# Kernel optimization log

Hardware: AMD Instinct MI355X
Metric: run time of the kernel (lower is better)

The kernel has to match this reference:

```python
import jax, jax.numpy as jnp
import numpy as np

TAU = 2.0
EPS = 1e-5
SG_ALPHA = 4.0  # spikingjelly default Sigmoid surrogate alpha


@jax.custom_vjp
def heaviside(x):
    return (x >= 0.0).astype(x.dtype)

def _heaviside_fwd(x):
    return heaviside(x), x

def _heaviside_bwd(x, g):
    s = jax.nn.sigmoid(SG_ALPHA * x)
    return (g * SG_ALPHA * s * (1.0 - s),)

heaviside.defvjp(_heaviside_fwd, _heaviside_bwd)


def lif(x_seq, v_th):
    """Multi-step LIF, hard reset to 0, detach_reset=True. x_seq: (T, ...)."""
    def step(v, x_t):
        v = v + (x_t - v) / TAU
        s = heaviside(v - v_th)
        v = v * (1.0 - jax.lax.stop_gradient(s))  # detached hard reset
        return v, s
    _, spikes = jax.lax.scan(step, jnp.zeros_like(x_seq[0]), x_seq)
    return spikes


def bn(y, gamma, beta, mean, var):
    # y: (T, B, C, N); inference-mode BatchNorm1d over channel dim
    inv = gamma / jnp.sqrt(var + EPS)
    return y * inv[None, None, :, None] + (beta - mean * inv)[None, None, :, None]


def setup_inputs() -> dict:
    key = jax.random.key(0)
    ks = jax.random.split(key, 8)
    T, B, C, H, W = 4, 32, 256, 32, 32
    d = {
        "x": jax.random.normal(ks[0], (T, B, C, H, W), jnp.float32),
        "q_w": jax.random.normal(ks[1], (C, C), jnp.float32) * (1.0 / np.sqrt(C)),
        "q_gamma": jnp.ones((C,), jnp.float32),
        "q_beta": jnp.zeros((C,), jnp.float32),
        "q_mean": jnp.zeros((C,), jnp.float32),
        "q_var": jnp.ones((C,), jnp.float32),
        "k_w": jax.random.normal(ks[2], (C, C), jnp.float32) * (1.0 / np.sqrt(C)),
        "k_gamma": jnp.ones((C,), jnp.float32),
        "k_beta": jnp.zeros((C,), jnp.float32),
        "k_mean": jnp.zeros((C,), jnp.float32),
        "k_var": jnp.ones((C,), jnp.float32),
        "p_w": jax.random.normal(ks[3], (C, C), jnp.float32) * (1.0 / np.sqrt(C)),
        "p_b": jnp.zeros((C,), jnp.float32),
        "p_gamma": jnp.ones((C,), jnp.float32),
        "p_beta": jnp.zeros((C,), jnp.float32),
        "p_mean": jnp.zeros((C,), jnp.float32),
        "p_var": jnp.ones((C,), jnp.float32),
    }
    return d


def reference(x, q_w, q_gamma, q_beta, q_mean, q_var,
              k_w, k_gamma, k_beta, k_mean, k_var,
              p_w, p_b, p_gamma, p_beta, p_mean, p_var):
    T, B, C, H, W = x.shape
    num_heads = 8
    dh = C // num_heads
    N = H * W
    xs = x.reshape(T, B, C, N)

    # Q branch: 1x1 conv (C x C matmul) -> BN -> LIF
    q = bn(jnp.einsum('oc,tbcn->tbon', q_w, xs), q_gamma, q_beta, q_mean, q_var)
    q_spikes = lif(q, 1.0)                                # (T,B,C,N)
    q_h = q_spikes.reshape(T, B, num_heads, dh, N)

    # K branch
    k = bn(jnp.einsum('oc,tbcn->tbon', k_w, xs), k_gamma, k_beta, k_mean, k_var)
    k_spikes = lif(k, 1.0)
    k_h = k_spikes.reshape(T, B, num_heads, dh, N)

    # channel-sum pooled Q per head -> attn LIF (v_th=0.5) -> elementwise mult with K
    q_sum = jnp.sum(q_h, axis=3, keepdims=True)           # (T,B,h,1,N)
    attn = lif(q_sum, 0.5)
    x_one = attn * k_h                                    # (T,B,h,dh,N)

    # projection: 1x1 conv with bias -> BN -> LIF
    xo = x_one.reshape(T, B, C, N)
    xo = jnp.einsum('oc,tbcn->tbon', p_w, xo) + p_b[None, None, :, None]
    xo = bn(xo, p_gamma, p_beta, p_mean, p_var).reshape(T, B, C, H, W)
    x_final = lif(xo, 1.0)
    return x_final
```

## Files before the change

kernel.cpp:

```cpp
#include <hip/hip_runtime.h>
#include <cstdint>
#include <cstddef>

#define T_DIM 4
#define B_DIM 32
#define C_DIM 256
#define N_DIM 1024
#define NHEAD 8
#define DHEAD 32
#define NWRD 32

__device__ __forceinline__ float lif_step(float& v, float x, float vth) {
    v = __fadd_rn(v, __fmul_rn(__fsub_rn(x, v), 0.5f));
    const float s = (v >= vth) ? 1.0f : 0.0f;
    if (s != 0.0f) v = 0.0f;
    return s;
}

__device__ __forceinline__ void async_copy16(const float* g, float* l) {
    __builtin_amdgcn_global_load_lds(
        (const __attribute__((address_space(1))) unsigned int*)g,
        (__attribute__((address_space(3))) unsigned int*)l, 16, 0, 0);
}

#define FMA_ROW(r, av)                                \
    acc[(r)*8+0] = fmaf(av, b0.x, acc[(r)*8+0]);      \
    acc[(r)*8+1] = fmaf(av, b0.y, acc[(r)*8+1]);      \
    acc[(r)*8+2] = fmaf(av, b0.z, acc[(r)*8+2]);      \
    acc[(r)*8+3] = fmaf(av, b0.w, acc[(r)*8+3]);      \
    acc[(r)*8+4] = fmaf(av, b1.x, acc[(r)*8+4]);      \
    acc[(r)*8+5] = fmaf(av, b1.y, acc[(r)*8+5]);      \
    acc[(r)*8+6] = fmaf(av, b1.z, acc[(r)*8+6]);      \
    acc[(r)*8+7] = fmaf(av, b1.w, acc[(r)*8+7]);

__global__ __launch_bounds__(256) void k_transpose(
    const float* __restrict__ qw, const float* __restrict__ kw,
    const float* __restrict__ pw, float* __restrict__ wqk_t,
    float* __restrict__ p_t)
{
    const int i = blockIdx.x * 256 + threadIdx.x;
    if (i < C_DIM * 512) {
        const int k = i >> 9, col = i & 511;
        const int h = col >> 6, j = col & 63;
        wqk_t[i] = (j < 32) ? qw[(size_t)(h * 32 + j) * C_DIM + k]
                            : kw[(size_t)(h * 32 + j - 32) * C_DIM + k];
    } else {
        const int i2 = i - C_DIM * 512;
        const int k = i2 >> 8, c = i2 & 255;
        p_t[i2] = pw[(size_t)c * C_DIM + k];
    }
}

__global__ __launch_bounds__(256, 4) void k_qk(
    const float* __restrict__ x, const float* __restrict__ wqk,
    const float* __restrict__ qg, const float* __restrict__ qbeta,
    const float* __restrict__ qmean, const float* __restrict__ qvar,
    const float* __restrict__ kg, const float* __restrict__ kbeta,
    const float* __restrict__ kmean, const float* __restrict__ kvar,
    uint32_t* __restrict__ xbits)
{
    __shared__ float w_lds[32 * 64];
    __shared__ float x_lds[32 * 128];
    float*    qsum_lds = x_lds;
    float*    attn_lds = x_lds + 128;
    uint32_t* pack_lds = (uint32_t*)(x_lds + 256);

    const int tid = threadIdx.x;
    const int h = blockIdx.x, nt = blockIdx.y, b = blockIdx.z;
    const int n0g = nt * 128;

    const int  mg = tid >> 4;
    const int  m0 = mg << 2;
    const int  ng = tid & 15;
    const int  n0 = ng << 2;
    const bool is_q = (mg < 8);

    float inv4[4], bias4[4];
    {
        const float* g  = is_q ? qg    : kg;
        const float* be = is_q ? qbeta : kbeta;
        const float* me = is_q ? qmean : kmean;
        const float* va = is_q ? qvar  : kvar;
        const int cb = h * DHEAD + (is_q ? m0 : (m0 - 32));
        #pragma unroll
        for (int i = 0; i < 4; i++) {
            const float iv = __fdiv_rn(g[cb + i], __fsqrt_rn(__fadd_rn(va[cb + i], 1e-5f)));
            inv4[i]  = iv;
            bias4[i] = __fsub_rn(be[cb + i], __fmul_rn(me[cb + i], iv));
        }
    }

    const int wk = tid >> 4;
    const int wm = (tid & 15) << 2;
    const int xk = tid >> 5;
    const int xc = (tid & 31) << 2;
    const float* wgp = wqk + h * 64 + wm;

    float vstate[32];
    #pragma unroll
    for (int i = 0; i < 32; i++) vstate[i] = 0.0f;
    float v_attn = 0.0f;

    for (int t = 0; t < T_DIM; ++t) {
        float acc[32];
        #pragma unroll
        for (int i = 0; i < 32; i++) acc[i] = 0.0f;

        const float* xgp = x + (size_t)(t * B_DIM + b) * C_DIM * N_DIM + n0g + xc;

        for (int c = 0; c < 8; ++c) {
            const int kk = c * 32;
            __syncthreads();
            async_copy16(wgp + (size_t)(kk      + wk) * 512, w_lds + tid * 4);
            async_copy16(wgp + (size_t)(kk + 16 + wk) * 512, w_lds + 1024 + tid * 4);
            #pragma unroll
            for (int r = 0; r < 4; r++)
                async_copy16(xgp + (size_t)(kk + r * 8 + xk) * N_DIM,
                             x_lds + r * 1024 + tid * 4);
            __syncthreads();
            #pragma unroll 4
            for (int k = 0; k < 32; k++) {
                const float4 a  = *(const float4*)(w_lds + k * 64 + m0);
                const float4 b0 = *(const float4*)(x_lds + k * 128 + n0);
                const float4 b1 = *(const float4*)(x_lds + k * 128 + 64 + n0);
                FMA_ROW(0, a.x)
                FMA_ROW(1, a.y)
                FMA_ROW(2, a.z)
                FMA_ROW(3, a.w)
            }
        }

        #pragma unroll
        for (int r = 0; r < 4; r++) {
            #pragma unroll
            for (int j = 0; j < 8; j++) {
                const float y = __fadd_rn(__fmul_rn(acc[r * 8 + j], inv4[r]), bias4[r]);
                acc[r * 8 + j] = lif_step(vstate[r * 8 + j], y, 1.0f);
            }
        }

        __syncthreads();
        if (tid < 128) qsum_lds[tid] = 0.0f; else pack_lds[tid - 128] = 0u;
        __syncthreads();

        if (is_q) {
            #pragma unroll
            for (int j = 0; j < 8; j++) {
                const int col = (j < 4) ? (n0 + j) : (64 + n0 + (j - 4));
                const float cs = acc[j] + acc[8 + j] + acc[16 + j] + acc[24 + j];
                atomicAdd(&qsum_lds[col], cs);
            }
        }
        __syncthreads();
        if (tid < 128) attn_lds[tid] = lif_step(v_attn, qsum_lds[tid], 0.5f);
        __syncthreads();

        if (!is_q) {
            #pragma unroll
            for (int r = 0; r < 4; r++) {
                const int krow = (mg - 8) * 4 + r;
                #pragma unroll
                for (int ci = 0; ci < 2; ci++) {
                    uint32_t nib = 0;
                    #pragma unroll
                    for (int jj = 0; jj < 4; jj++) {
                        const int col = ci * 64 + n0 + jj;
                        if (acc[r * 8 + ci * 4 + jj] != 0.0f && attn_lds[col] != 0.0f)
                            nib |= (1u << jj);
                    }
                    if (nib) {
                        const int word = ci * 2 + (ng >> 3);
                        const int shf  = (ng & 7) * 4;
                        atomicOr(&pack_lds[krow * 4 + word], nib << shf);
                    }
                }
            }
        }
        __syncthreads();
        if (tid < 128) {
            const int krow = tid >> 2, word = tid & 3;
            const int ch = h * DHEAD + krow;
            xbits[((size_t)(t * B_DIM + b) * C_DIM + ch) * NWRD + nt * 4 + word]
                = pack_lds[tid];
        }
    }
}

__global__ __launch_bounds__(256, 4) void k_proj(
    const uint32_t* __restrict__ xbits, const float* __restrict__ pt,
    const float* __restrict__ pbias, const float* __restrict__ pg,
    const float* __restrict__ pbeta, const float* __restrict__ pmean,
    const float* __restrict__ pvar, float* __restrict__ out)
{
    __shared__ float w_lds[32 * 64];
    __shared__ float x_lds[32 * 128];

    const int tid = threadIdx.x;
    const int mt = blockIdx.x, nt = blockIdx.y, b = blockIdx.z;
    const int n0g = nt * 128;
    const int c0  = mt * 64;

    const int mg = tid >> 4, m0 = mg << 2;
    const int ng = tid & 15, n0 = ng << 2;

    float inv4[4], bias4[4], pb4[4];
    #pragma unroll
    for (int i = 0; i < 4; i++) {
        const int ch = c0 + m0 + i;
        const float iv = __fdiv_rn(pg[ch], __fsqrt_rn(__fadd_rn(pvar[ch], 1e-5f)));
        inv4[i]  = iv;
        bias4[i] = __fsub_rn(pbeta[ch], __fmul_rn(pmean[ch], iv));
        pb4[i]   = pbias[ch];
    }

    const int wk = tid >> 4;
    const int wm = (tid & 15) << 2;
    const float* wgp = pt + c0 + wm;

    const int usel = nt * 4 + ((tid & 31) >> 3);
    const int shf  = (tid & 7) * 4;
    const int urow = tid >> 5;

    float vstate[32];
    #pragma unroll
    for (int i = 0; i < 32; i++) vstate[i] = 0.0f;

    for (int t = 0; t < T_DIM; ++t) {
        float acc[32];
        #pragma unroll
        for (int i = 0; i < 32; i++) acc[i] = 0.0f;

        const uint32_t* xg = xbits + (size_t)(t * B_DIM + b) * C_DIM * NWRD;

        uint32_t u[4];
        #pragma unroll
        for (int r = 0; r < 4; r++)
            u[r] = xg[(size_t)(r * 8 + urow) * NWRD + usel];

        for (int c = 0; c < 8; ++c) {
            __syncthreads();
            #pragma unroll
            for (int r = 0; r < 4; r++) {
                const uint32_t bits = (u[r] >> shf) & 0xFu;
                float4 f;
                f.x = (bits & 1u)        ? 1.0f : 0.0f;
                f.y = ((bits >> 1) & 1u) ? 1.0f : 0.0f;
                f.z = ((bits >> 2) & 1u) ? 1.0f : 0.0f;
                f.w = ((bits >> 3) & 1u) ? 1.0f : 0.0f;
                *(float4*)(x_lds + r * 1024 + tid * 4) = f;
            }
            async_copy16(wgp + (size_t)(c * 32      + wk) * 256, w_lds + tid * 4);
            async_copy16(wgp + (size_t)(c * 32 + 16 + wk) * 256, w_lds + 1024 + tid * 4);
            __syncthreads();
            if (c + 1 < 8) {
                #pragma unroll
                for (int r = 0; r < 4; r++)
                    u[r] = xg[(size_t)((c + 1) * 32 + r * 8 + urow) * NWRD + usel];
            }
            #pragma unroll 4
            for (int k = 0; k < 32; k++) {
                const float4 a  = *(const float4*)(w_lds + k * 64 + m0);
                const float4 b0 = *(const float4*)(x_lds + k * 128 + n0);
                const float4 b1 = *(const float4*)(x_lds + k * 128 + 64 + n0);
                FMA_ROW(0, a.x)
                FMA_ROW(1, a.y)
                FMA_ROW(2, a.z)
                FMA_ROW(3, a.w)
            }
        }

        #pragma unroll
        for (int r = 0; r < 4; r++) {
            const int ch = c0 + m0 + r;
            float* ob = out + ((size_t)(t * B_DIM + b) * C_DIM + ch) * N_DIM + n0g;
            float4 oA, oB;
            float oAv[4], oBv[4];
            #pragma unroll
            for (int j = 0; j < 8; j++) {
                float y = __fadd_rn(acc[r * 8 + j], pb4[r]);
                y = __fadd_rn(__fmul_rn(y, inv4[r]), bias4[r]);
                const float s = lif_step(vstate[r * 8 + j], y, 1.0f);
                if (j < 4) oAv[j] = s; else oBv[j - 4] = s;
            }
            oA.x = oAv[0]; oA.y = oAv[1]; oA.z = oAv[2]; oA.w = oAv[3];
            oB.x = oBv[0]; oB.y = oBv[1]; oB.z = oBv[2]; oB.w = oBv[3];
            *(float4*)(ob + n0)      = oA;
            *(float4*)(ob + 64 + n0) = oB;
        }
    }
}

extern "C" void kernel_launch(void* const* d_in, const int* in_sizes, int n_in,
                              void* d_out, int out_size, void* d_ws, size_t ws_size,
                              hipStream_t stream) {
    const float* x    = (const float*)d_in[0];
    const float* q_w  = (const float*)d_in[1];
    const float* q_g  = (const float*)d_in[2];
    const float* q_b  = (const float*)d_in[3];
    const float* q_m  = (const float*)d_in[4];
    const float* q_v  = (const float*)d_in[5];
    const float* k_w  = (const float*)d_in[6];
    const float* k_g  = (const float*)d_in[7];
    const float* k_b  = (const float*)d_in[8];
    const float* k_m  = (const float*)d_in[9];
    const float* k_v  = (const float*)d_in[10];
    const float* p_w  = (const float*)d_in[11];
    const float* p_b  = (const float*)d_in[12];
    const float* p_g  = (const float*)d_in[13];
    const float* p_be = (const float*)d_in[14];
    const float* p_m  = (const float*)d_in[15];
    const float* p_v  = (const float*)d_in[16];

    float*    wqk_t = (float*)d_ws;
    float*    p_t   = (float*)((char*)d_ws + 524288);
    uint32_t* xbits = (uint32_t*)((char*)d_ws + 786432);
    float*    out   = (float*)d_out;

    k_transpose<<<768, 256, 0, stream>>>(q_w, k_w, p_w, wqk_t, p_t);

    dim3 g1(NHEAD, N_DIM / 128, B_DIM);
    k_qk<<<g1, 256, 0, stream>>>(x, wqk_t, q_g, q_b, q_m, q_v,
                                 k_g, k_b, k_m, k_v, xbits);

    dim3 g2(C_DIM / 64, N_DIM / 128, B_DIM);
    k_proj<<<g2, 256, 0, stream>>>(xbits, p_t, p_b, p_g, p_be, p_m, p_v, out);
}
```

Measured before the change: 877.6 us.

## Enlarge register tiles to 8x8 per thread, processing two heads per block

Each thread's micro-tile grows from 4x8 to 8x8 outputs in both the QK and projection GEMM kernels, so each block covers 128 output channels (two heads in k_qk) and the grid is halved. The goal is better arithmetic intensity per LDS load and fewer redundant reloads of x tiles across head blocks. BN constants move to shared memory, and the bit-unpack loader in k_proj is reorganised around the new tile. The cost is much higher register pressure (64 accumulators plus 64 LIF states), occupancy lowered to 3 blocks per SM, and fewer blocks in the grid.

Measured after the change: 829.0 us. 1.06x faster.

```diff
diff --git a/kernel.cpp b/kernel.cpp
--- a/kernel.cpp
+++ b/kernel.cpp
@@ -32,6 +32,16 @@
     acc[(r)*8+5] = fmaf(av, b1.y, acc[(r)*8+5]);      \
     acc[(r)*8+6] = fmaf(av, b1.z, acc[(r)*8+6]);      \
     acc[(r)*8+7] = fmaf(av, b1.w, acc[(r)*8+7]);
+
+#define FMA_8x8()        \
+    FMA_ROW(0, a0.x)     \
+    FMA_ROW(1, a0.y)     \
+    FMA_ROW(2, a0.z)     \
+    FMA_ROW(3, a0.w)     \
+    FMA_ROW(4, a1.x)     \
+    FMA_ROW(5, a1.y)     \
+    FMA_ROW(6, a1.z)     \
+    FMA_ROW(7, a1.w)
 
 __global__ __launch_bounds__(256) void k_transpose(
     const float* __restrict__ qw, const float* __restrict__ kw,
@@ -51,7 +61,7 @@
     }
 }
 
-__global__ __launch_bounds__(256, 4) void k_qk(
+__global__ __launch_bounds__(256, 3) void k_qk(
     const float* __restrict__ x, const float* __restrict__ wqk,
     const float* __restrict__ qg, const float* __restrict__ qbeta,
     const float* __restrict__ qmean, const float* __restrict__ qvar,
@@ -59,229 +69,237 @@
     const float* __restrict__ kmean, const float* __restrict__ kvar,
     uint32_t* __restrict__ xbits)
 {
-    __shared__ float w_lds[32 * 64];
+    __shared__ float w_lds[32 * 128];
     __shared__ float x_lds[32 * 128];
+    __shared__ float inv_lds[128];
+    __shared__ float bias_lds[128];
     float*    qsum_lds = x_lds;
-    float*    attn_lds = x_lds + 128;
-    uint32_t* pack_lds = (uint32_t*)(x_lds + 256);
+    float*    attn_lds = x_lds + 256;
+    uint32_t* pack_lds = (uint32_t*)(x_lds + 512);
 
     const int tid = threadIdx.x;
-    const int h = blockIdx.x, nt = blockIdx.y, b = blockIdx.z;
+    const int hp = blockIdx.x, nt = blockIdx.y, b = blockIdx.z;
     const int n0g = nt * 128;
 
-    const int  mg = tid >> 4;
-    const int  m0 = mg << 2;
-    const int  ng = tid & 15;
-    const int  n0 = ng << 2;
-    const bool is_q = (mg < 8);
-
-    float inv4[4], bias4[4];
-    {
-        const float* g  = is_q ? qg    : kg;
-        const float* be = is_q ? qbeta : kbeta;
-        const float* me = is_q ? qmean : kmean;
-        const float* va = is_q ? qvar  : kvar;
-        const int cb = h * DHEAD + (is_q ? m0 : (m0 - 32));
+    const int  mg   = tid >> 4;
+    const int  m0   = mg << 3;
+    const int  ng   = tid & 15;
+    const int  n0   = ng << 2;
+    const int  hsel = mg >> 3;
+    const bool is_q = ((mg & 7) < 4);
+
+    if (tid < 128) {
+        const int m = tid;
+        const int hs = m >> 6, j = m & 63;
+        const int h = hp * 2 + hs;
+        const bool q = (j < 32);
+        const float* g  = q ? qg    : kg;
+        const float* be = q ? qbeta : kbeta;
+        const float* me = q ? qmean : kmean;
+        const float* va = q ? qvar  : kvar;
+        const int ch = h * DHEAD + (q ? j : j - 32);
+        const float iv = __fdiv_rn(g[ch], __fsqrt_rn(__fadd_rn(va[ch], 1e-5f)));
+        inv_lds[m]  = iv;
+        bias_lds[m] = __fsub_rn(be[ch], __fmul_rn(me[ch], iv));
+    }
+
+    const int skl  = tid >> 5;
+    const int scol = (tid & 31) << 2;
+    const float* wgp = wqk + (size_t)skl * 512 + hp * 128 + scol;
+
+    float vstate[64];
+    #pragma unroll
+    for (int i = 0; i < 64; i++) vstate[i] = 0.0f;
+    float v_attn = 0.0f;
+
+    for (int t = 0; t < T_DIM; ++t) {
+        float acc[64];
         #pragma unroll
-        for (int i = 0; i < 4; i++) {
-            const float iv = __fdiv_rn(g[cb + i], __fsqrt_rn(__fadd_rn(va[cb + i], 1e-5f)));
-            inv4[i]  = iv;
-            bias4[i] = __fsub_rn(be[cb + i], __fmul_rn(me[cb + i], iv));
-        }
-    }
-
-    const int wk = tid >> 4;
-    const int wm = (tid & 15) << 2;
-    const int xk = tid >> 5;
-    const int xc = (tid & 31) << 2;
-    const float* wgp = wqk + h * 64 + wm;
-
-    float vstate[32];
-    #pragma unroll
-    for (int i = 0; i < 32; i++) vstate[i] = 0.0f;
-    float v_attn = 0.0f;
-
-    for (int t = 0; t < T_DIM; ++t) {
-        float acc[32];
-        #pragma unroll
-        for (int i = 0; i < 32; i++) acc[i] = 0.0f;
-
-        const float* xgp = x + (size_t)(t * B_DIM + b) * C_DIM * N_DIM + n0g + xc;
+        for (int i = 0; i < 64; i++) acc[i] = 0.0f;
+
+        const float* xgp = x + ((size_t)(t * B_DIM + b) * C_DIM + skl) * N_DIM
+                           + n0g + scol;
 
         for (int c = 0; c < 8; ++c) {
             const int kk = c * 32;
             __syncthreads();
-            async_copy16(wgp + (size_t)(kk      + wk) * 512, w_lds + tid * 4);
-            async_copy16(wgp + (size_t)(kk + 16 + wk) * 512, w_lds + 1024 + tid * 4);
-            #pragma unroll
-            for (int r = 0; r < 4; r++)
-                async_copy16(xgp + (size_t)(kk + r * 8 + xk) * N_DIM,
-                             x_lds + r * 1024 + tid * 4);
+            #pragma unroll
+            for (int r = 0; r < 4; r++) {
+                async_copy16(wgp + (size_t)(kk + r * 8) * 512, w_lds + r * 1024 + tid * 4);
+                async_copy16(xgp + (size_t)(kk + r * 8) * N_DIM, x_lds + r * 1024 + tid * 4);
+            }
             __syncthreads();
-            #pragma unroll 4
+            #pragma unroll 2
             for (int k = 0; k < 32; k++) {
-                const float4 a  = *(const float4*)(w_lds + k * 64 + m0);
+                const float4 a0 = *(const float4*)(w_lds + k * 128 + m0);
+                const float4 a1 = *(const float4*)(w_lds + k * 128 + m0 + 4);
                 const float4 b0 = *(const float4*)(x_lds + k * 128 + n0);
                 const float4 b1 = *(const float4*)(x_lds + k * 128 + 64 + n0);
-                FMA_ROW(0, a.x)
-                FMA_ROW(1, a.y)
-                FMA_ROW(2, a.z)
-                FMA_ROW(3, a.w)
+                FMA_8x8()
             }
         }
 
         #pragma unroll
-        for (int r = 0; r < 4; r++) {
+        for (int r = 0; r < 8; r++) {
+            const float iv = inv_lds[m0 + r];
+            const float bs = bias_lds[m0 + r];
             #pragma unroll
             for (int j = 0; j < 8; j++) {
-                const float y = __fadd_rn(__fmul_rn(acc[r * 8 + j], inv4[r]), bias4[r]);
+                const float y = __fadd_rn(__fmul_rn(acc[r * 8 + j], iv), bs);
                 acc[r * 8 + j] = lif_step(vstate[r * 8 + j], y, 1.0f);
             }
         }
 
         __syncthreads();
-        if (tid < 128) qsum_lds[tid] = 0.0f; else pack_lds[tid - 128] = 0u;
+        qsum_lds[tid] = 0.0f;
+        pack_lds[tid] = 0u;
         __syncthreads();
 
         if (is_q) {
             #pragma unroll
             for (int j = 0; j < 8; j++) {
                 const int col = (j < 4) ? (n0 + j) : (64 + n0 + (j - 4));
-                const float cs = acc[j] + acc[8 + j] + acc[16 + j] + acc[24 + j];
-                atomicAdd(&qsum_lds[col], cs);
-            }
-        }
-        __syncthreads();
-        if (tid < 128) attn_lds[tid] = lif_step(v_attn, qsum_lds[tid], 0.5f);
+                float cs = acc[j];
+                #pragma unroll
+                for (int r = 1; r < 8; r++) cs += acc[r * 8 + j];
+                atomicAdd(&qsum_lds[hsel * 128 + col], cs);
+            }
+        }
+        __syncthreads();
+        attn_lds[tid] = lif_step(v_attn, qsum_lds[tid], 0.5f);
         __syncthreads();
 
         if (!is_q) {
             #pragma unroll
-            for (int r = 0; r < 4; r++) {
-                const int krow = (mg - 8) * 4 + r;
+            for (int r = 0; r < 8; r++) {
+                const int krow = ((mg & 7) - 4) * 8 + r;
                 #pragma unroll
                 for (int ci = 0; ci < 2; ci++) {
                     uint32_t nib = 0;
                     #pragma unroll
                     for (int jj = 0; jj < 4; jj++) {
                         const int col = ci * 64 + n0 + jj;
-                        if (acc[r * 8 + ci * 4 + jj] != 0.0f && attn_lds[col] != 0.0f)
+                        if (acc[r * 8 + ci * 4 + jj] != 0.0f &&
+                            attn_lds[hsel * 128 + col] != 0.0f)
                             nib |= (1u << jj);
                     }
                     if (nib) {
                         const int word = ci * 2 + (ng >> 3);
                         const int shf  = (ng & 7) * 4;
-                        atomicOr(&pack_lds[krow * 4 + word], nib << shf);
+                        atomicOr(&pack_lds[hsel * 128 + krow * 4 + word], nib << shf);
                     }
                 }
             }
         }
         __syncthreads();
-        if (tid < 128) {
-            const int krow = tid >> 2, word = tid & 3;
-            const int ch = h * DHEAD + krow;
+        {
+            const int hs2  = tid >> 7;
+            const int rem  = tid & 127;
+            const int krow = rem >> 2, word = rem & 3;
+            const int ch = (hp * 2 + hs2) * DHEAD + krow;
             xbits[((size_t)(t * B_DIM + b) * C_DIM + ch) * NWRD + nt * 4 + word]
                 = pack_lds[tid];
         }
     }
 }
 
-__global__ __launch_bounds__(256, 4) void k_proj(
+__global__ __launch_bounds__(256, 3) void k_proj(
     const uint32_t* __restrict__ xbits, const float* __restrict__ pt,
     const float* __restrict__ pbias, const float* __restrict__ pg,
     const float* __restrict__ pbeta, const float* __restrict__ pmean,
     const float* __restrict__ pvar, float* __restrict__ out)
 {
-    __shared__ float w_lds[32 * 64];
+    __shared__ float w_lds[32 * 128];
     __shared__ float x_lds[32 * 128];
+    __shared__ float inv_lds[128];
+    __shared__ float bias_lds[128];
+    __shared__ float pb_lds[128];
 
     const int tid = threadIdx.x;
     const int mt = blockIdx.x, nt = blockIdx.y, b = blockIdx.z;
     const int n0g = nt * 128;
-    const int c0  = mt * 64;
-
-    const int mg = tid >> 4, m0 = mg << 2;
+    const int c0  = mt * 128;
+
+    const int mg = tid >> 4, m0 = mg << 3;
     const int ng = tid & 15, n0 = ng << 2;
 
-    float inv4[4], bias4[4], pb4[4];
+    if (tid < 128) {
+        const int ch = c0 + tid;
+        const float iv = __fdiv_rn(pg[ch], __fsqrt_rn(__fadd_rn(pvar[ch], 1e-5f)));
+        inv_lds[tid]  = iv;
+        bias_lds[tid] = __fsub_rn(pbeta[ch], __fmul_rn(pmean[ch], iv));
+        pb_lds[tid]   = pbias[ch];
+    }
+
+    const int skl  = tid >> 5;
+    const int scol = (tid & 31) << 2;
+    const float* wgp = pt + (size_t)skl * 256 + c0 + scol;
+
+    const int urow = tid >> 3, cg = tid & 7;
+    const int wsel = nt * 4 + (cg >> 1);
+    const int ushf = (cg & 1) * 16;
+    float* xw = x_lds + tid * 16;
+
+    float vstate[64];
     #pragma unroll
-    for (int i = 0; i < 4; i++) {
-        const int ch = c0 + m0 + i;
-        const float iv = __fdiv_rn(pg[ch], __fsqrt_rn(__fadd_rn(pvar[ch], 1e-5f)));
-        inv4[i]  = iv;
-        bias4[i] = __fsub_rn(pbeta[ch], __fmul_rn(pmean[ch], iv));
-        pb4[i]   = pbias[ch];
-    }
-
-    const int wk = tid >> 4;
-    const int wm = (tid & 15) << 2;
-    const float* wgp = pt + c0 + wm;
-
-    const int usel = nt * 4 + ((tid & 31) >> 3);
-    const int shf  = (tid & 7) * 4;
-    const int urow = tid >> 5;
-
-    float vstate[32];
-    #pragma unroll
-    for (int i = 0; i < 32; i++) vstate[i] = 0.0f;
+    for (int i = 0; i < 64; i++) vstate[i] = 0.0f;
 
     for (int t = 0; t < T_DIM; ++t) {
-        float acc[32];
+        float acc[64];
         #pragma unroll
-        for (int i = 0; i < 32; i++) acc[i] = 0.0f;
+        for (int i = 0; i < 64; i++) acc[i] = 0.0f;
 
         const uint32_t* xg = xbits + (size_t)(t * B_DIM + b) * C_DIM * NWRD;
 
-        uint32_t u[4];
-        #pragma unroll
-        for (int r = 0; r < 4; r++)
-            u[r] = xg[(size_t)(r * 8 + urow) * NWRD + usel];
+        uint32_t u = xg[(size_t)urow * NWRD + wsel];
 
         for (int c = 0; c < 8; ++c) {
             __syncthreads();
-            #pragma unroll
-            for (int r = 0; r < 4; r++) {
-                const uint32_t bits = (u[r] >> shf) & 0xFu;
-                float4 f;
-                f.x = (bits & 1u)        ? 1.0f : 0.0f;
-                f.y = ((bits >> 1) & 1u) ? 1.0f : 0.0f;
-                f.z = ((bits >> 2) & 1u) ? 1.0f : 0.0f;
-                f.w = ((bits >> 3) & 1u) ? 1.0f : 0.0f;
-                *(float4*)(x_lds + r * 1024 + tid * 4) = f;
-            }
-            async_copy16(wgp + (size_t)(c * 32      + wk) * 256, w_lds + tid * 4);
-            async_copy16(wgp + (size_t)(c * 32 + 16 + wk) * 256, w_lds + 1024 + tid * 4);
+            {
+                const uint32_t bits = (u >> ushf) & 0xffffu;
+                #pragma unroll
+                for (int q4 = 0; q4 < 4; q4++) {
+                    float4 f;
+                    f.x = ((bits >> (q4 * 4 + 0)) & 1u) ? 1.0f : 0.0f;
+                    f.y = ((bits >> (q4 * 4 + 1)) & 1u) ? 1.0f : 0.0f;
+                    f.z = ((bits >> (q4 * 4 + 2)) & 1u) ? 1.0f : 0.0f;
+                    f.w = ((bits >> (q4 * 4 + 3)) & 1u) ? 1.0f : 0.0f;
+                    *(float4*)(xw + q4 * 4) = f;
+                }
+            }
+            #pragma unroll
+            for (int r = 0; r < 4; r++)
+                async_copy16(wgp + (size_t)(c * 32 + r * 8) * 256,
+                             w_lds + r * 1024 + tid * 4);
             __syncthreads();
-            if (c + 1 < 8) {
-                #pragma unroll
-                for (int r = 0; r < 4; r++)
-                    u[r] = xg[(size_t)((c + 1) * 32 + r * 8 + urow) * NWRD + usel];
-            }
-            #pragma unroll 4
+            if (c + 1 < 8)
+                u = xg[(size_t)((c + 1) * 32 + urow) * NWRD + wsel];
+            #pragma unroll 2
             for (int k = 0; k < 32; k++) {
-                const float4 a  = *(const float4*)(w_lds + k * 64 + m0);
+                const float4 a0 = *(const float4*)(w_lds + k * 128 + m0);
+                const float4 a1 = *(const float4*)(w_lds + k * 128 + m0 + 4);
                 const float4 b0 = *(const float4*)(x_lds + k * 128 + n0);
                 const float4 b1 = *(const float4*)(x_lds + k * 128 + 64 + n0);
-                FMA_ROW(0, a.x)
-                FMA_ROW(1, a.y)
-                FMA_ROW(2, a.z)
-                FMA_ROW(3, a.w)
+                FMA_8x8()
             }
         }
 
         #pragma unroll
-        for (int r = 0; r < 4; r++) {
+        for (int r = 0; r < 8; r++) {
             const int ch = c0 + m0 + r;
+            const float iv = inv_lds[m0 + r];
+            const float bs = bias_lds[m0 + r];
+            const float pb = pb_lds[m0 + r];
             float* ob = out + ((size_t)(t * B_DIM + b) * C_DIM + ch) * N_DIM + n0g;
-            float4 oA, oB;
             float oAv[4], oBv[4];
             #pragma unroll
             for (int j = 0; j < 8; j++) {
-                float y = __fadd_rn(acc[r * 8 + j], pb4[r]);
-                y = __fadd_rn(__fmul_rn(y, inv4[r]), bias4[r]);
+                float y = __fadd_rn(acc[r * 8 + j], pb);
+                y = __fadd_rn(__fmul_rn(y, iv), bs);
                 const float s = lif_step(vstate[r * 8 + j], y, 1.0f);
                 if (j < 4) oAv[j] = s; else oBv[j - 4] = s;
             }
+            float4 oA, oB;
             oA.x = oAv[0]; oA.y = oAv[1]; oA.z = oAv[2]; oA.w = oAv[3];
             oB.x = oBv[0]; oB.y = oBv[1]; oB.z = oBv[2]; oB.w = oBv[3];
             *(float4*)(ob + n0)      = oA;
@@ -318,10 +336,10 @@
 
     k_transpose<<<768, 256, 0, stream>>>(q_w, k_w, p_w, wqk_t, p_t);
 
-    dim3 g1(NHEAD, N_DIM / 128, B_DIM);
+    dim3 g1(NHEAD / 2, N_DIM / 128, B_DIM);
     k_qk<<<g1, 256, 0, stream>>>(x, wqk_t, q_g, q_b, q_m, q_v,
                                  k_g, k_b, k_m, k_v, xbits);
 
-    dim3 g2(C_DIM / 64, N_DIM / 128, B_DIM);
+    dim3 g2(C_DIM / 128, N_DIM / 128, B_DIM);
     k_proj<<<g2, 256, 0, stream>>>(xbits, p_t, p_b, p_g, p_be, p_m, p_v, out);
 }
```
